# Performance work log

Measured on AMD Instinct MI355X. Metric: run time of the kernel, lower is better.

## Reference

```python
import jax, jax.numpy as jnp
import numpy as np

EPS = 1e-5
TOPK = 4

def bn(x, gamma, beta, mean, var, axis=1):
    # inference-mode batchnorm (running stats)
    shp = [1] * x.ndim
    shp[axis] = -1
    scale = (gamma / jnp.sqrt(var + EPS)).reshape(shp)
    shift = (beta - mean * gamma / jnp.sqrt(var + EPS)).reshape(shp)
    return x * scale + shift


def setup_inputs() -> dict:
    key = jax.random.key(0)
    ks = jax.random.split(key, 4)
    B, C, T, H, W = 8, 512, 8, 28, 28
    R = 64
    Cq = C // 4
    s = 0.05
    return {
        "input": jax.random.normal(ks[0], (B, C, T, H, W), dtype=jnp.float32),
        "w_reduce": jax.random.normal(ks[1], (R, C), dtype=jnp.float32) * s,
        "bn1_gamma": jnp.ones((R,), jnp.float32), "bn1_beta": jnp.zeros((R,), jnp.float32),
        "bn1_mean": jnp.zeros((R,), jnp.float32), "bn1_var": jnp.ones((R,), jnp.float32),
        "w_proj": jax.random.normal(ks[2], (Cq, C + 2), dtype=jnp.float32) * s,
        "bn2_gamma": jnp.ones((Cq,), jnp.float32), "bn2_beta": jnp.zeros((Cq,), jnp.float32),
        "bn2_mean": jnp.zeros((Cq,), jnp.float32), "bn2_var": jnp.ones((Cq,), jnp.float32),
        "w_t": jax.random.normal(ks[3], (C, Cq, 3, 1), dtype=jnp.float32) * s,
        "bn3_gamma": jnp.ones((C,), jnp.float32), "bn3_beta": jnp.zeros((C,), jnp.float32),
        "bn3_mean": jnp.zeros((C,), jnp.float32), "bn3_var": jnp.ones((C,), jnp.float32),
    }


def reference(input, w_reduce, bn1_gamma, bn1_beta, bn1_mean, bn1_var,
              w_proj, bn2_gamma, bn2_beta, bn2_mean, bn2_var,
              w_t, bn3_gamma, bn3_beta, bn3_mean, bn3_var):
    x = input
    B, C, T, H, W = x.shape
    R = w_reduce.shape[0]
    K = TOPK
    HW = H * W

    # spatial template from frame 0
    template_d = x[:, :, 0].reshape(B, C, HW)                                  # (B,C,HW)
    template_p = bn(jnp.einsum('rc,bcs->brs', w_reduce, template_d),
                    bn1_gamma, bn1_beta, bn1_mean, bn1_var)                     # (B,R,HW)
    spt_inds = jnp.argmax(template_p, axis=2)                                  # (B,R)
    template_resample = jnp.take_along_axis(template_d, spt_inds[:, None, :], axis=2)  # (B,C,R)

    x_flat = x.reshape(B, C, T * HW)
    affinity = jnp.einsum('bcr,bcs->brs', template_resample, x_flat)           # (B,R,T*HW)
    affinity = affinity.reshape(B, R, T, HW)
    _, topk_inds = jax.lax.top_k(affinity, K)                                  # (B,R,T,K)
    inds = jnp.transpose(topk_inds, (0, 3, 2, 1))                              # (B,K,T,R)

    # gather trajectory features: traj[b,k,c,t,r] = x[b,c,t, inds[b,k,t,r]]
    x4 = x.reshape(B, C, T, HW)
    traj = jnp.take_along_axis(x4[:, None], inds[:, :, None], axis=4)          # (B,K,C,T,R)
    traj_bk = traj.reshape(B * K, C, T, R)

    inds_bk = inds.reshape(B * K, 1, T, R)
    row = (inds_bk // W).astype(jnp.float32) / H
    col = (inds_bk % W).astype(jnp.float32) / W
    coords = jnp.concatenate([row, col], axis=1)                               # (B*K,2,T,R)

    fuse = jnp.concatenate([traj_bk, coords], axis=1)                          # (B*K,C+2,T,R)
    fuse = bn(jnp.einsum('qc,bctr->bqtr', w_proj, fuse),
              bn2_gamma, bn2_beta, bn2_mean, bn2_var)                          # (B*K,C/4,T,R)
    fuse = fuse.reshape(B, K, C // 4, T, R).max(axis=1)                        # (B,C/4,T,R)

    tc = jax.lax.conv_general_dilated(fuse, w_t, window_strides=(1, 1),
                                      padding=((1, 1), (0, 0)),
                                      dimension_numbers=('NCHW', 'OIHW', 'NCHW'))
    tc = jax.nn.relu(bn(tc, bn3_gamma, bn3_beta, bn3_mean, bn3_var))           # (B,C,T,R)

    points = traj.mean(axis=1).reshape(B, C, T * R)                            # (B,C,T*R)
    proj = jnp.einsum('bcp,bcs->bps', points, x_flat)                          # (B,T*R,T*HW)
    proj = jax.nn.softmax(proj, axis=1)                                        # softmax over T*R (dim=1)
    prop = jnp.einsum('bcp,bps->bcs', tc.reshape(B, C, T * R), proj)           # (B,C,T*HW)
    return x + prop.reshape(B, C, T, H, W)
```

## Files before the change

### kernel.cpp

```cpp
#include <hip/hip_runtime.h>

#define EPSB 1e-5f

#define B_   8
#define C_   512
#define T_   8
#define HW_  784
#define S_   6272
#define R_   64
#define CQ_  128
#define K_   4
#define P_   512

typedef _Float16 f16;
typedef __attribute__((ext_vector_type(8))) _Float16 f16x8;
typedef __attribute__((ext_vector_type(4))) _Float16 f16x4;
typedef __attribute__((ext_vector_type(4))) float    f32x4;

#define OB_PTST  0ull
#define OB_TC    4194304ull
#define OB_D     8388608ull
#define OB_TRH   8589312ull
#define OB_TRF   9113600ull
#define OB_INDS  10162176ull
#define OB_WRH   10227712ull
#define OB_WPH   10293248ull
#define OB_WTH   10424320ull
#define OB_XT    10817536ull
#define T_TPA    62197760ull
#define T_AFF    63803392ull
#define T_FUSEK  62197760ull
#define T_FUSE   66392064ull
#define CHB      62197760ull

#define SBAR()  __builtin_amdgcn_s_barrier()
#define SCHB()  __builtin_amdgcn_sched_barrier(0)
#define WAITV(N) asm volatile("s_waitcnt vmcnt(" #N ")" ::: "memory")

__device__ __forceinline__ void gload16(const void* g, void* l) {
    __builtin_amdgcn_global_load_lds(
        (const __attribute__((address_space(1))) unsigned int*)g,
        (__attribute__((address_space(3))) unsigned int*)l, 16, 0, 0);
}

__global__ __launch_bounds__(256) void k_prep(
    const float* __restrict__ wr, const float* __restrict__ wp,
    const float* __restrict__ wt,
    f16* __restrict__ wrh, f16* __restrict__ wph, f16* __restrict__ wth)
{
    int i = blockIdx.x*256 + threadIdx.x;
    if (i < 32768) {
        wrh[i] = (f16)wr[i];
    } else if (i < 98304) {
        int j = i - 32768;
        int q = j >> 9, c = j & 511;
        wph[j] = (f16)wp[q*514 + c];
    } else {
        int j = i - 98304;
        int co = j / 384;
        int rem = j - co*384;
        int dt = rem >> 7, ci = rem & 127;
        wth[j] = (f16)wt[(size_t)(co*CQ_ + ci)*3 + dt];
    }
}

__global__ __launch_bounds__(256) void k_xpose(
    const float* __restrict__ x, f16* __restrict__ xT)
{
    __shared__ float tile[64][65];
    int s0 = blockIdx.x*64, c0 = blockIdx.y*64, b = blockIdx.z;
    int tid = threadIdx.x;
    #pragma unroll
    for (int i = 0; i < 4; ++i) {
        int idx = tid + i*256;
        int cl = idx >> 4, s4 = (idx & 15)*4;
        f32x4 v = *(const f32x4*)&x[((size_t)(b*C_ + c0+cl))*S_ + s0 + s4];
        tile[cl][s4] = v.x; tile[cl][s4+1] = v.y;
        tile[cl][s4+2] = v.z; tile[cl][s4+3] = v.w;
    }
    __syncthreads();
    #pragma unroll
    for (int i = 0; i < 4; ++i) {
        int idx = tid + i*256;
        int sl = idx >> 4, c4 = (idx & 15)*4;
        f16x4 h;
        h[0] = (f16)tile[c4+0][sl]; h[1] = (f16)tile[c4+1][sl];
        h[2] = (f16)tile[c4+2][sl]; h[3] = (f16)tile[c4+3][sl];
        *(f16x4*)&xT[((size_t)(b*S_ + s0+sl))*C_ + c0 + c4] = h;
    }
}

__global__ __launch_bounds__(256) void k_templ(
    const f16* __restrict__ xT, const f16* __restrict__ wrh,
    float* __restrict__ tpa)
{
    __shared__ __align__(16) f16 As[2][128*64];
    __shared__ __align__(16) f16 Bs[2][64*64];
    int b = blockIdx.y; int s0 = blockIdx.x*128;
    int tid = threadIdx.x;
    int lane = tid & 63, w = tid >> 6;
    int lrow = lane >> 3;
    int swzc = ((lane & 7) ^ lrow) * 8;
    const f16* ga = xT  + ((size_t)b*S_ + s0 + w*32 + lrow)*C_ + swzc;
    const f16* gb = wrh + (size_t)(w*16 + lrow)*C_ + swzc;
    int mbase = (w & 1)*64, nbase = (w >> 1)*32;
    int fr = lane & 15, quad = lane >> 4;
    int sw = fr & 7;
    f32x4 acc[4][2] = {};
    #pragma unroll
    for (int j = 0; j < 4; ++j)
        gload16(ga + j*8*C_, &As[0][(w*32 + j*8)*64]);
    #pragma unroll
    for (int j = 0; j < 2; ++j)
        gload16(gb + j*8*C_, &Bs[0][(w*16 + j*8)*64]);
    ga += 64; gb += 64;
    int cur = 0;
    for (int i = 0; i < 8; ++i) {
        if (i < 7) {
            #pragma unroll
            for (int j = 0; j < 4; ++j)
                gload16(ga + j*8*C_, &As[cur^1][(w*32 + j*8)*64]);
            #pragma unroll
            for (int j = 0; j < 2; ++j)
                gload16(gb + j*8*C_, &Bs[cur^1][(w*16 + j*8)*64]);
            ga += 64; gb += 64;
            WAITV(6);
        } else {
            WAITV(0);
        }
        SCHB(); SBAR();
        #pragma unroll
        for (int kk = 0; kk < 2; ++kk) {
            int ch = ((kk*4 + quad) ^ sw) * 8;
            f16x8 af[4], bf[2];
            #pragma unroll
            for (int mt = 0; mt < 4; ++mt)
                af[mt] = *(const f16x8*)&As[cur][(mbase + mt*16 + fr)*64 + ch];
            #pragma unroll
            for (int nt = 0; nt < 2; ++nt)
                bf[nt] = *(const f16x8*)&Bs[cur][(nbase + nt*16 + fr)*64 + ch];
            #pragma unroll
            for (int mt = 0; mt < 4; ++mt)
                #pragma unroll
                for (int nt = 0; nt < 2; ++nt)
                    acc[mt][nt] = __builtin_amdgcn_mfma_f32_16x16x32_f16(
                        af[mt], bf[nt], acc[mt][nt], 0, 0, 0);
        }
        SBAR();
        cur ^= 1;
    }
    #pragma unroll
    for (int mt = 0; mt < 4; ++mt) {
        int sb = s0 + mbase + mt*16 + quad*4;
        if (sb < HW_) {
            #pragma unroll
            for (int nt = 0; nt < 2; ++nt) {
                int r = nbase + nt*16 + fr;
                *(f32x4*)&tpa[((size_t)(b*R_ + r))*HW_ + sb] = acc[mt][nt];
            }
        }
    }
}

__global__ __launch_bounds__(256) void k_targmax(
    const float* __restrict__ x, const float* __restrict__ wr_g,
    const float* __restrict__ g1, const float* __restrict__ v1,
    const float* __restrict__ tpa,
    float* __restrict__ trf, f16* __restrict__ trh)
{
    __shared__ float row[HW_];
    __shared__ float sval[256];
    __shared__ int   sidx[256];
    __shared__ float cval[4];
    __shared__ int   cidx[4];
    __shared__ float eval_[4];
    __shared__ int   bestind;
    int bid = blockIdx.x;
    int b = bid >> 6, r = bid & 63;
    int tid = threadIdx.x;
    float sc = g1[r] * rsqrtf(v1[r] + EPSB);
    const float* tprow = tpa + (size_t)bid*HW_;
    for (int s = tid; s < HW_; s += 256) row[s] = tprow[s]*sc;
    __syncthreads();
    for (int pass = 0; pass < 4; ++pass) {
        float best = -INFINITY; int bi = 0;
        for (int s = tid; s < HW_; s += 256) {
            float v = row[s];
            if (v > best) { best = v; bi = s; }
        }
        sval[tid] = best; sidx[tid] = bi;
        __syncthreads();
        for (int off = 128; off > 0; off >>= 1) {
            if (tid < off) {
                float ov = sval[tid+off]; int oi = sidx[tid+off];
                if (ov > sval[tid] || (ov == sval[tid] && oi < sidx[tid])) {
                    sval[tid] = ov; sidx[tid] = oi;
                }
            }
            __syncthreads();
        }
        if (tid == 0) {
            cval[pass] = sval[0]; cidx[pass] = sidx[0];
            row[sidx[0]] = -INFINITY;
        }
        __syncthreads();
    }
    float thr = 0.05f * fabsf(sc);
    if (cval[0] - cval[1] >= thr) {
        if (tid == 0) bestind = cidx[0];
    } else {
        int w = tid >> 6, lane = tid & 63;
        int cand = cidx[w];
        float sum = 0.f;
        #pragma unroll
        for (int i = 0; i < 8; ++i) {
            int c = lane + i*64;
            sum += wr_g[r*C_ + c] * x[((size_t)(b*C_ + c))*S_ + cand];
        }
        #pragma unroll
        for (int off = 32; off > 0; off >>= 1) sum += __shfl_xor(sum, off);
        if (lane == 0) eval_[w] = sum*sc;
        __syncthreads();
        if (tid == 0) {
            float bv = eval_[0]; int bi2 = cidx[0];
            for (int j = 1; j < 4; ++j) {
                float v = eval_[j]; int ii = cidx[j];
                if (v > bv || (v == bv && ii < bi2)) { bv = v; bi2 = ii; }
            }
            bestind = bi2;
        }
    }
    __syncthreads();
    int ind = bestind;
    for (int c = tid; c < C_; c += 256) {
        float v = x[((size_t)(b*C_ + c))*S_ + ind];
        trf[(size_t)bid*C_ + c] = v;
        trh[(size_t)bid*C_ + c] = (f16)v;
    }
}

__global__ __launch_bounds__(256) void k_affin(
    const f16* __restrict__ xT, const f16* __restrict__ trh,
    float* __restrict__ aff)
{
    __shared__ __align__(16) f16 As[2][128*64];
    __shared__ __align__(16) f16 Bs[2][64*64];
    int b = blockIdx.y; int s0 = blockIdx.x*128;
    int tid = threadIdx.x;
    int lane = tid & 63, w = tid >> 6;
    int lrow = lane >> 3;
    int swzc = ((lane & 7) ^ lrow) * 8;
    const f16* ga = xT  + ((size_t)b*S_ + s0 + w*32 + lrow)*C_ + swzc;
    const f16* gb = trh + ((size_t)(b*R_) + w*16 + lrow)*C_ + swzc;
    int mbase = (w & 1)*64, nbase = (w >> 1)*32;
    int fr = lane & 15, quad = lane >> 4;
    int sw = fr & 7;
    f32x4 acc[4][2] = {};
    #pragma unroll
    for (int j = 0; j < 4; ++j)
        gload16(ga + j*8*C_, &As[0][(w*32 + j*8)*64]);
    #pragma unroll
    for (int j = 0; j < 2; ++j)
        gload16(gb + j*8*C_, &Bs[0][(w*16 + j*8)*64]);
    ga += 64; gb += 64;
    int cur = 0;
    for (int i = 0; i < 8; ++i) {
        if (i < 7) {
            #pragma unroll
            for (int j = 0; j < 4; ++j)
                gload16(ga + j*8*C_, &As[cur^1][(w*32 + j*8)*64]);
            #pragma unroll
            for (int j = 0; j < 2; ++j)
                gload16(gb + j*8*C_, &Bs[cur^1][(w*16 + j*8)*64]);
            ga += 64; gb += 64;
            WAITV(6);
        } else {
            WAITV(0);
        }
        SCHB(); SBAR();
        #pragma unroll
        for (int kk = 0; kk < 2; ++kk) {
            int ch = ((kk*4 + quad) ^ sw) * 8;
            f16x8 af[4], bf[2];
            #pragma unroll
            for (int mt = 0; mt < 4; ++mt)
                af[mt] = *(const f16x8*)&As[cur][(mbase + mt*16 + fr)*64 + ch];
            #pragma unroll
            for (int nt = 0; nt < 2; ++nt)
                bf[nt] = *(const f16x8*)&Bs[cur][(nbase + nt*16 + fr)*64 + ch];
            #pragma unroll
            for (int mt = 0; mt < 4; ++mt)
                #pragma unroll
                for (int nt = 0; nt < 2; ++nt)
                    acc[mt][nt] = __builtin_amdgcn_mfma_f32_16x16x32_f16(
                        af[mt], bf[nt], acc[mt][nt], 0, 0, 0);
        }
        SBAR();
        cur ^= 1;
    }
    #pragma unroll
    for (int mt = 0; mt < 4; ++mt) {
        int sb = s0 + mbase + mt*16 + quad*4;
        #pragma unroll
        for (int nt = 0; nt < 2; ++nt) {
            int r = nbase + nt*16 + fr;
            *(f32x4*)&aff[((size_t)(b*R_ + r))*S_ + sb] = acc[mt][nt];
        }
    }
}

__global__ __launch_bounds__(256) void k_topk(
    const float* __restrict__ x, const float* __restrict__ trf,
    const float* __restrict__ aff, int* __restrict__ inds)
{
    __shared__ float row[HW_];
    __shared__ float sval[256];
    __shared__ int   sidx[256];
    __shared__ float cval[8];
    __shared__ int   cidx[8];
    __shared__ float eval_[8];
    int r = blockIdx.x, t = blockIdx.y, b = blockIdx.z;
    int tid = threadIdx.x;
    const float* arow = aff + ((size_t)(b*R_ + r))*S_ + t*HW_;
    for (int s = tid; s < HW_; s += 256) row[s] = arow[s];
    __syncthreads();
    for (int pass = 0; pass < 8; ++pass) {
        float best = -INFINITY; int bi = 0;
        for (int s = tid; s < HW_; s += 256) {
            float v = row[s];
            if (v > best) { best = v; bi = s; }
        }
        sval[tid] = best; sidx[tid] = bi;
        __syncthreads();
        for (int off = 128; off > 0; off >>= 1) {
            if (tid < off) {
                float ov = sval[tid+off]; int oi = sidx[tid+off];
                if (ov > sval[tid] || (ov == sval[tid] && oi < sidx[tid])) {
                    sval[tid] = ov; sidx[tid] = oi;
                }
            }
            __syncthreads();
        }
        if (tid == 0) {
            cval[pass] = sval[0]; cidx[pass] = sidx[0];
            row[sidx[0]] = -INFINITY;
        }
        __syncthreads();
    }
    if (cval[3] - cval[4] >= 0.35f) {
        if (tid < K_)
            inds[((b*K_ + tid)*T_ + t)*R_ + r] = cidx[tid];
    } else {
        int w = tid >> 6, lane = tid & 63;
        #pragma unroll
        for (int half = 0; half < 2; ++half) {
            int j = w + half*4;
            int cand = cidx[j];
            float sum = 0.f;
            #pragma unroll
            for (int i = 0; i < 8; ++i) {
                int c = lane + i*64;
                sum += trf[((size_t)(b*R_ + r))*C_ + c]
                     * x[((size_t)(b*C_ + c))*S_ + t*HW_ + cand];
            }
            #pragma unroll
            for (int off = 32; off > 0; off >>= 1) sum += __shfl_xor(sum, off);
            if (lane == 0) eval_[j] = sum;
        }
        __syncthreads();
        if (tid == 0) {
            unsigned used = 0;
            for (int k = 0; k < K_; ++k) {
                float bv = -INFINITY; int bj = -1;
                for (int j = 0; j < 8; ++j) {
                    if (used & (1u << j)) continue;
                    float v = eval_[j]; int ii = cidx[j];
                    if (bj < 0 || v > bv || (v == bv && ii < cidx[bj])) {
                        bv = v; bj = j;
                    }
                }
                used |= 1u << bj;
                inds[((b*K_ + k)*T_ + t)*R_ + r] = cidx[bj];
            }
        }
    }
}

__global__ __launch_bounds__(256) void k_pointsT(
    const float* __restrict__ x, const int* __restrict__ inds,
    f16* __restrict__ ptsT)
{
    __shared__ float tile[64][65];
    __shared__ int   indl[4][64];
    int c0 = blockIdx.x*64, t = blockIdx.y, b = blockIdx.z;
    int tid = threadIdx.x;
    {
        int k = tid >> 6, r = tid & 63;
        indl[k][r] = inds[((b*K_ + k)*T_ + t)*R_ + r];
    }
    __syncthreads();
    #pragma unroll
    for (int i = 0; i < 16; ++i) {
        int idx = tid + i*256;
        int cl = idx >> 6, r = idx & 63;
        const float* base = x + (size_t)(b*C_ + c0 + cl)*S_ + t*HW_;
        float v = base[indl[0][r]] + base[indl[1][r]] + base[indl[2][r]] + base[indl[3][r]];
        tile[cl][r] = 0.25f*v;
    }
    __syncthreads();
    #pragma unroll
    for (int i = 0; i < 16; ++i) {
        int idx = tid + i*256;
        int rl = idx >> 6, cl = idx & 63;
        ptsT[((size_t)b*P_ + t*64 + rl)*C_ + c0 + cl] = (f16)tile[cl][rl];
    }
}

__global__ __launch_bounds__(256) void k_fuse(
    const f16* __restrict__ xT, const f16* __restrict__ wph,
    const float* __restrict__ wp,
    const float* __restrict__ g2, const float* __restrict__ b2,
    const float* __restrict__ m2, const float* __restrict__ v2,
    f16* __restrict__ fusekT, const int* __restrict__ inds)
{
    __shared__ __align__(16) f16 As[2][128*32];
    __shared__ __align__(16) f16 Bs[2][64*32];
    __shared__ float scq[128], shq[128], wrq[128], wcq[128];
    __shared__ float rowv[64], colv[64];
    int bid = blockIdx.x;
    int t = bid & 7, bk = bid >> 3;
    int b = bk >> 2;
    int tid = threadIdx.x;
    int lane = tid & 63, w = tid >> 6;
    if (tid < 128) {
        float sc = g2[tid] * rsqrtf(v2[tid] + EPSB);
        scq[tid] = sc;
        shq[tid] = b2[tid] - m2[tid]*sc;
        wrq[tid] = wp[tid*514 + 512];
        wcq[tid] = wp[tid*514 + 513];
    } else if (tid < 192) {
        int r = tid - 128;
        int id = inds[bk*T_*R_ + t*R_ + r];
        rowv[r] = (float)(id / 28) * (1.0f/28.0f);
        colv[r] = (float)(id % 28) * (1.0f/28.0f);
    }
    int strow = tid >> 2;
    int slot  = (tid & 3) ^ (strow & 3);
    int ind = inds[bk*T_*R_ + t*R_ + strow];
    const f16* ga = wph + (size_t)strow*C_ + slot*8;
    const f16* gb = xT + ((size_t)b*S_ + t*HW_ + ind)*C_ + slot*8;
    int mbase = (w & 1)*64, nbase = (w >> 1)*32;
    int fr = lane & 15, quad = lane >> 4;
    f32x4 acc[4][2] = {};
    __syncthreads();
    gload16(ga,         (f16*)As[0] + tid*8);
    gload16(ga + 64*C_, (f16*)As[0] + 2048 + tid*8);
    gload16(gb,         (f16*)Bs[0] + tid*8);
    ga += 32; gb += 32;
    int cur = 0;
    for (int i = 0; i < 16; ++i) {
        if (i < 15) {
            gload16(ga,         (f16*)As[cur^1] + tid*8);
            gload16(ga + 64*C_, (f16*)As[cur^1] + 2048 + tid*8);
            gload16(gb,         (f16*)Bs[cur^1] + tid*8);
            ga += 32; gb += 32;
            WAITV(3);
        } else {
            WAITV(0);
        }
        SCHB(); SBAR();
        f16x8 af[4], bf[2];
        #pragma unroll
        for (int mt = 0; mt < 4; ++mt) {
            int ar = mbase + mt*16 + fr;
            af[mt] = *(const f16x8*)&As[cur][ar*32 + ((quad ^ (ar & 3))*8)];
        }
        #pragma unroll
        for (int nt = 0; nt < 2; ++nt) {
            int br = nbase + nt*16 + fr;
            bf[nt] = *(const f16x8*)&Bs[cur][br*32 + ((quad ^ (br & 3))*8)];
        }
        #pragma unroll
        for (int mt = 0; mt < 4; ++mt)
            #pragma unroll
            for (int nt = 0; nt < 2; ++nt)
                acc[mt][nt] = __builtin_amdgcn_mfma_f32_16x16x32_f16(
                    af[mt], bf[nt], acc[mt][nt], 0, 0, 0);
        SBAR();
        cur ^= 1;
    }
    #pragma unroll
    for (int mt = 0; mt < 4; ++mt) {
        int qb = mbase + mt*16 + quad*4;
        #pragma unroll
        for (int nt = 0; nt < 2; ++nt) {
            int r = nbase + nt*16 + fr;
            f16x4 h;
            #pragma unroll
            for (int i = 0; i < 4; ++i) {
                int q = qb + i;
                float v = acc[mt][nt][i] + wrq[q]*rowv[r] + wcq[q]*colv[r];
                h[i] = (f16)(v*scq[q] + shq[q]);
            }
            *(f16x4*)&fusekT[((size_t)bk*P_ + t*R_ + r)*CQ_ + qb] = h;
        }
    }
}

__global__ __launch_bounds__(256) void k_maxk(
    const f16* __restrict__ fusekT, f16* __restrict__ fuseT)
{
    int idx8 = (blockIdx.x*256 + threadIdx.x)*8;
    int b = idx8 >> 16;
    int pq = idx8 & 65535;
    const f16* base = fusekT + (size_t)(b*4)*65536 + pq;
    f16x8 v0 = *(const f16x8*)base;
    #pragma unroll
    for (int k = 1; k < K_; ++k) {
        f16x8 vk = *(const f16x8*)(base + (size_t)k*65536);
        #pragma unroll
        for (int j = 0; j < 8; ++j)
            v0[j] = (float)vk[j] > (float)v0[j] ? vk[j] : v0[j];
    }
    *(f16x8*)&fuseT[(size_t)b*65536 + pq] = v0;
}

__global__ __launch_bounds__(256) void k_conv(
    const f16* __restrict__ wth,
    const float* __restrict__ g3, const float* __restrict__ b3,
    const float* __restrict__ m3, const float* __restrict__ v3,
    const f16* __restrict__ fuseT, f16* __restrict__ tc)
{
    __shared__ __align__(16) f16 As[128*64];
    __shared__ __align__(16) f16 Bs[128*64];
    int p0 = blockIdx.x*128, c0 = blockIdx.y*128, b = blockIdx.z;
    int tid = threadIdx.x;
    int lane = tid & 63, w = tid >> 6;
    int lrow = lane >> 3;
    int swzc = ((lane & 7) ^ lrow) * 8;
    int mrow = (w & 1)*64, nrow = (w >> 1)*64;
    int fr = lane & 15, quad = lane >> 4;
    int sw = fr & 7;
    f32x4 acc[4][4] = {};
    for (int step = 0; step < 6; ++step) {
        int dt = step >> 1, h = step & 1;
        int shift = (dt - 1)*64;
        #pragma unroll
        for (int j = 0; j < 4; ++j) {
            int rb = w*32 + j*8;
            int pg = p0 + rb + shift;
            if (pg >= 0 && pg < P_)
                gload16(fuseT + ((size_t)b*P_ + pg + lrow)*CQ_ + h*64 + swzc,
                        &As[rb*64]);
            else
                *(f32x4*)((char*)&As[rb*64] + lane*16) = (f32x4){0.f,0.f,0.f,0.f};
        }
        #pragma unroll
        for (int j = 0; j < 4; ++j) {
            int rb = w*32 + j*8;
            gload16(wth + (size_t)(c0 + rb + lrow)*384 + dt*128 + h*64 + swzc,
                    &Bs[rb*64]);
        }
        __syncthreads();
        #pragma unroll
        for (int kk = 0; kk < 2; ++kk) {
            int ch = ((kk*4 + quad) ^ sw) * 8;
            f16x8 af[4], bf[4];
            #pragma unroll
            for (int mt = 0; mt < 4; ++mt)
                af[mt] = *(const f16x8*)&As[(mrow + mt*16 + fr)*64 + ch];
            #pragma unroll
            for (int nt = 0; nt < 4; ++nt)
                bf[nt] = *(const f16x8*)&Bs[(nrow + nt*16 + fr)*64 + ch];
            #pragma unroll
            for (int mt = 0; mt < 4; ++mt)
                #pragma unroll
                for (int nt = 0; nt < 4; ++nt)
                    acc[mt][nt] = __builtin_amdgcn_mfma_f32_16x16x32_f16(
                        af[mt], bf[nt], acc[mt][nt], 0, 0, 0);
        }
        __syncthreads();
    }
    #pragma unroll
    for (int nt = 0; nt < 4; ++nt) {
        int co = c0 + nrow + nt*16 + fr;
        float sc = g3[co] * rsqrtf(v3[co] + EPSB);
        float sh = b3[co] - m3[co]*sc;
        #pragma unroll
        for (int mt = 0; mt < 4; ++mt) {
            int p = p0 + mrow + mt*16 + quad*4;
            f16x4 hv;
            #pragma unroll
            for (int i = 0; i < 4; ++i)
                hv[i] = (f16)fmaxf(acc[mt][nt][i]*sc + sh, 0.f);
            *(f16x4*)&tc[((size_t)(b*C_ + co))*P_ + p] = hv;
        }
    }
}

__global__ __launch_bounds__(512, 2) void k_attnW(
    const f16* __restrict__ xT, const f16* __restrict__ ptsT,
    f16* __restrict__ W, float* __restrict__ Dinv, int st, int NCHb)
{
    __shared__ __align__(16) f16 As[2][128*32];
    __shared__ __align__(16) f16 Bs[2][512*32];
    int lt = blockIdx.x; int b = blockIdx.z;
    int s0 = (st + lt)*128;
    int tid = threadIdx.x;
    int lane = tid & 63, w = tid >> 6;
    int wr = w & 1, wc = w >> 1;
    int strow = tid >> 2;
    int slot  = (tid & 3) ^ (strow & 3);
    const f16* ga = xT   + ((size_t)b*S_ + s0 + strow)*C_ + slot*8;
    const f16* gb = ptsT + ((size_t)b*P_ + strow)*C_ + slot*8;
    int fr = lane & 15, quad = lane >> 4;
    f32x4 acc[8][4] = {};
    gload16(ga, (f16*)As[0] + tid*8);
    #pragma unroll
    for (int j = 0; j < 4; ++j)
        gload16(gb + (size_t)j*128*C_, (f16*)Bs[0] + j*4096 + tid*8);
    ga += 32; gb += 32;
    int cur = 0;
    for (int i = 0; i < 16; ++i) {
        if (i < 15) {
            gload16(ga, (f16*)As[cur^1] + tid*8);
            #pragma unroll
            for (int j = 0; j < 4; ++j)
                gload16(gb + (size_t)j*128*C_, (f16*)Bs[cur^1] + j*4096 + tid*8);
            ga += 32; gb += 32;
            WAITV(5);
        } else {
            WAITV(0);
        }
        SCHB(); SBAR();
        f16x8 af[4], bf[8];
        #pragma unroll
        for (int mt = 0; mt < 4; ++mt) {
            int ar = wr*64 + mt*16 + fr;
            af[mt] = *(const f16x8*)&As[cur][ar*32 + ((quad ^ (ar & 3))*8)];
        }
        #pragma unroll
        for (int nt = 0; nt < 8; ++nt) {
            int br = wc*128 + nt*16 + fr;
            bf[nt] = *(const f16x8*)&Bs[cur][br*32 + ((quad ^ (br & 3))*8)];
        }
        #pragma unroll
        for (int nt = 0; nt < 8; ++nt)
            #pragma unroll
            for (int mt = 0; mt < 4; ++mt)
                acc[nt][mt] = __builtin_amdgcn_mfma_f32_16x16x32_f16(
                    bf[nt], af[mt], acc[nt][mt], 0, 0, 0);
        SBAR();
        cur ^= 1;
    }
    float (*red)[4] = (float (*)[4])As;
    float M[4];
    #pragma unroll
    for (int mt = 0; mt < 4; ++mt) {
        float m = -INFINITY;
        #pragma unroll
        for (int nt = 0; nt < 8; ++nt)
            #pragma unroll
            for (int i = 0; i < 4; ++i)
                m = fmaxf(m, acc[nt][mt][i]);
        m = fmaxf(m, __shfl_xor(m, 16));
        m = fmaxf(m, __shfl_xor(m, 32));
        if (quad == 0) red[wr*64 + mt*16 + fr][wc] = m;
    }
    __syncthreads();
    #pragma unroll
    for (int mt = 0; mt < 4; ++mt) {
        int srow = wr*64 + mt*16 + fr;
        M[mt] = fmaxf(fmaxf(red[srow][0], red[srow][1]),
                      fmaxf(red[srow][2], red[srow][3]));
    }
    __syncthreads();
    #pragma unroll
    for (int mt = 0; mt < 4; ++mt) {
        float s = 0.f;
        #pragma unroll
        for (int nt = 0; nt < 8; ++nt)
            #pragma unroll
            for (int i = 0; i < 4; ++i) {
                float e = __expf(acc[nt][mt][i] - M[mt]);
                acc[nt][mt][i] = e;
                s += e;
            }
        s += __shfl_xor(s, 16);
        s += __shfl_xor(s, 32);
        if (quad == 0) red[wr*64 + mt*16 + fr][wc] = s;
    }
    __syncthreads();
    size_t wbase = (size_t)(b*NCHb + lt)*128*(size_t)P_;
    #pragma unroll
    for (int mt = 0; mt < 4; ++mt) {
        int srow = wr*64 + mt*16 + fr;
        float tot = (red[srow][0] + red[srow][1]) + (red[srow][2] + red[srow][3]);
        if (wc == 0 && quad == 0)
            Dinv[(size_t)b*S_ + s0 + srow] = 1.0f/tot;
        #pragma unroll
        for (int nt = 0; nt < 8; ++nt) {
            f16x4 h;
            #pragma unroll
            for (int i = 0; i < 4; ++i) h[i] = (f16)acc[nt][mt][i];
            *(f16x4*)&W[wbase + (size_t)srow*P_ + wc*128 + nt*16 + quad*4] = h;
        }
    }
}

__global__ __launch_bounds__(256) void k_gemmP(
    const f16* __restrict__ tc, const f16* __restrict__ W,
    const float* __restrict__ Dinv, const float* __restrict__ x,
    float* __restrict__ out, int st, int NCHb)
{
    __shared__ __align__(16) f16 As[2][128*64];
    __shared__ __align__(16) f16 Bs[2][128*64];
    int lt = blockIdx.x; int b = blockIdx.z;
    int s0 = (st + lt)*128, c0t = blockIdx.y*128;
    int tid = threadIdx.x;
    int lane = tid & 63, w = tid >> 6;
    int lrow = lane >> 3;
    int swzc = ((lane & 7) ^ lrow) * 8;
    const f16* ga = tc + ((size_t)(b*C_) + c0t + w*32 + lrow)*P_ + swzc;
    const f16* gb = W  + ((size_t)(b*NCHb + lt)*128 + w*32 + lrow)*P_ + swzc;
    int mrow = (w & 1)*64, nrow = (w >> 1)*64;
    int fr = lane & 15, quad = lane >> 4;
    int sw = fr & 7;
    f32x4 acc[4][4] = {};
    #pragma unroll
    for (int j = 0; j < 4; ++j)
        gload16(ga + j*8*P_, &As[0][(w*32 + j*8)*64]);
    #pragma unroll
    for (int j = 0; j < 4; ++j)
        gload16(gb + j*8*P_, &Bs[0][(w*32 + j*8)*64]);
    ga += 64; gb += 64;
    int cur = 0;
    for (int i = 0; i < 8; ++i) {
        if (i < 7) {
            #pragma unroll
            for (int j = 0; j < 4; ++j)
                gload16(ga + j*8*P_, &As[cur^1][(w*32 + j*8)*64]);
            #pragma unroll
            for (int j = 0; j < 4; ++j)
                gload16(gb + j*8*P_, &Bs[cur^1][(w*32 + j*8)*64]);
            ga += 64; gb += 64;
            WAITV(8);
        } else {
            WAITV(0);
        }
        SCHB(); SBAR();
        #pragma unroll
        for (int kk = 0; kk < 2; ++kk) {
            int ch = ((kk*4 + quad) ^ sw) * 8;
            f16x8 af[4], bf[4];
            #pragma unroll
            for (int mt = 0; mt < 4; ++mt)
                af[mt] = *(const f16x8*)&As[cur][(mrow + mt*16 + fr)*64 + ch];
            #pragma unroll
            for (int nt = 0; nt < 4; ++nt)
                bf[nt] = *(const f16x8*)&Bs[cur][(nrow + nt*16 + fr)*64 + ch];
            #pragma unroll
            for (int nt = 0; nt < 4; ++nt)
                #pragma unroll
                for (int mt = 0; mt < 4; ++mt)
                    acc[nt][mt] = __builtin_amdgcn_mfma_f32_16x16x32_f16(
                        bf[nt], af[mt], acc[nt][mt], 0, 0, 0);
        }
        SBAR();
        cur ^= 1;
    }
    #pragma unroll
    for (int nt = 0; nt < 4; ++nt) {
        int s = s0 + nrow + nt*16 + quad*4;
        f32x4 dv = *(const f32x4*)&Dinv[(size_t)b*S_ + s];
        #pragma unroll
        for (int mt = 0; mt < 4; ++mt) {
            int c = c0t + mrow + mt*16 + fr;
            size_t o = ((size_t)(b*C_ + c))*S_ + s;
            f32x4 xv = *(const f32x4*)&x[o];
            f32x4 res = xv + acc[nt][mt]*dv;
            *(f32x4*)&out[o] = res;
        }
    }
}

extern "C" void kernel_launch(void* const* d_in, const int* in_sizes, int n_in,
                              void* d_out, int out_size, void* d_ws, size_t ws_size,
                              hipStream_t stream) {
    const float* x   = (const float*)d_in[0];
    const float* wrd = (const float*)d_in[1];
    const float* g1  = (const float*)d_in[2];
    const float* v1  = (const float*)d_in[5];
    const float* wp  = (const float*)d_in[6];
    const float* g2  = (const float*)d_in[7];
    const float* b2  = (const float*)d_in[8];
    const float* m2  = (const float*)d_in[9];
    const float* v2  = (const float*)d_in[10];
    const float* wt  = (const float*)d_in[11];
    const float* g3  = (const float*)d_in[12];
    const float* b3  = (const float*)d_in[13];
    const float* m3  = (const float*)d_in[14];
    const float* v3  = (const float*)d_in[15];
    char*  wsb = (char*)d_ws;
    float* out = (float*)d_out;

    f16*   ptsT  = (f16*)  (wsb + OB_PTST);
    f16*   tc    = (f16*)  (wsb + OB_TC);
    float* Dinv  = (float*)(wsb + OB_D);
    f16*   trh   = (f16*)  (wsb + OB_TRH);
    float* trf   = (float*)(wsb + OB_TRF);
    int*   inds  = (int*)  (wsb + OB_INDS);
    f16*   wrh   = (f16*)  (wsb + OB_WRH);
    f16*   wph   = (f16*)  (wsb + OB_WPH);
    f16*   wth   = (f16*)  (wsb + OB_WTH);
    f16*   xT    = (f16*)  (wsb + OB_XT);
    float* tpa   = (float*)(wsb + T_TPA);
    float* aff   = (float*)(wsb + T_AFF);
    f16*   fusekT= (f16*)  (wsb + T_FUSEK);
    f16*   fuseT = (f16*)  (wsb + T_FUSE);

    const size_t PER_TILE = 1048576ull;
    size_t avail = ws_size > CHB ? ws_size - CHB : 0;
    int NCH = (int)(avail / PER_TILE);
    if (NCH < 1) NCH = 1;
    if (NCH > 49) NCH = 49;
    int nchunks = (49 + NCH - 1)/NCH;
    int NCHb = (49 + nchunks - 1)/nchunks;
    f16* W = (f16*)(wsb + CHB);

    k_prep<<<1152, 256, 0, stream>>>(wrd, wp, wt, wrh, wph, wth);
    k_xpose<<<dim3(98, 8, 8), 256, 0, stream>>>(x, xT);
    k_templ<<<dim3(7, 8), 256, 0, stream>>>(xT, wrh, tpa);
    k_targmax<<<512, 256, 0, stream>>>(x, wrd, g1, v1, tpa, trf, trh);
    k_affin<<<dim3(49, 8), 256, 0, stream>>>(xT, trh, aff);
    k_topk<<<dim3(R_, T_, B_), 256, 0, stream>>>(x, trf, aff, inds);
    k_pointsT<<<dim3(8, 8, 8), 256, 0, stream>>>(x, inds, ptsT);
    k_fuse<<<256, 256, 0, stream>>>(xT, wph, wp, g2, b2, m2, v2, fusekT, inds);
    k_maxk<<<256, 256, 0, stream>>>(fusekT, fuseT);
    k_conv<<<dim3(4, 4, 8), 256, 0, stream>>>(wth, g3, b3, m3, v3, fuseT, tc);

    for (int st = 0; st < 49; st += NCHb) {
        int cnt = (49 - st) < NCHb ? (49 - st) : NCHb;
        k_attnW<<<dim3(cnt, 1, 8), 512, 0, stream>>>(xT, ptsT, W, Dinv, st, NCHb);
        k_gemmP<<<dim3(cnt, 4, 8), 256, 0, stream>>>(tc, W, Dinv, x, out, st, NCHb);
    }
}
```

Measured before the change: 480.4 us.

## Fuse softmax-weight and propagation GEMMs into one kernel keeping weights in LDS

Merges the attention-weight kernel and the propagation GEMM into a single kernel. Each block computes its 128x512 softmax weight tile, keeps it in about 147KB of LDS with a swizzled layout, then loops over all 512 channels multiplying by streamed tc tiles and writing x + prop. This removes the global round trip of the f16 weight matrix and the normalizer array, along with the chunked launch loop. In exchange only 392 blocks run at one block per CU because of the LDS footprint, so occupancy drops and the second GEMM uses small 2x2 MFMA tiles per wave.

```diff
diff --git a/kernel.cpp b/kernel.cpp
--- a/kernel.cpp
+++ b/kernel.cpp
@@ -31,7 +31,6 @@
 #define T_AFF    63803392ull
 #define T_FUSEK  62197760ull
 #define T_FUSE   66392064ull
-#define CHB      62197760ull
 
 #define SBAR()  __builtin_amdgcn_s_barrier()
 #define SCHB()  __builtin_amdgcn_sched_barrier(0)
@@ -598,188 +597,190 @@
     }
 }
 
-__global__ __launch_bounds__(512, 2) void k_attnW(
+__global__ __launch_bounds__(512, 2) void k_attnP(
     const f16* __restrict__ xT, const f16* __restrict__ ptsT,
-    f16* __restrict__ W, float* __restrict__ Dinv, int st, int NCHb)
-{
-    __shared__ __align__(16) f16 As[2][128*32];
-    __shared__ __align__(16) f16 Bs[2][512*32];
-    int lt = blockIdx.x; int b = blockIdx.z;
-    int s0 = (st + lt)*128;
+    const f16* __restrict__ tc, const float* __restrict__ x,
+    float* __restrict__ out)
+{
+    __shared__ __align__(16) char ldsb[150016];
+    f16*  P1A  = (f16*)ldsb;
+    f16*  P1B  = (f16*)(ldsb + 16384);
+    f16*  Wl   = (f16*)ldsb;
+    f16*  TCs  = (f16*)(ldsb + 131072);
+    float* dinv = (float*)(ldsb + 147456);
+    float (*red)[4] = (float (*)[4])(ldsb + 147968);
+
+    int lt = blockIdx.x, b = blockIdx.y;
+    int s0 = lt*128;
     int tid = threadIdx.x;
     int lane = tid & 63, w = tid >> 6;
     int wr = w & 1, wc = w >> 1;
-    int strow = tid >> 2;
-    int slot  = (tid & 3) ^ (strow & 3);
-    const f16* ga = xT   + ((size_t)b*S_ + s0 + strow)*C_ + slot*8;
-    const f16* gb = ptsT + ((size_t)b*P_ + strow)*C_ + slot*8;
     int fr = lane & 15, quad = lane >> 4;
-    f32x4 acc[8][4] = {};
-    gload16(ga, (f16*)As[0] + tid*8);
-    #pragma unroll
-    for (int j = 0; j < 4; ++j)
-        gload16(gb + (size_t)j*128*C_, (f16*)Bs[0] + j*4096 + tid*8);
-    ga += 32; gb += 32;
-    int cur = 0;
-    for (int i = 0; i < 16; ++i) {
-        if (i < 15) {
-            gload16(ga, (f16*)As[cur^1] + tid*8);
-            #pragma unroll
-            for (int j = 0; j < 4; ++j)
-                gload16(gb + (size_t)j*128*C_, (f16*)Bs[cur^1] + j*4096 + tid*8);
-            ga += 32; gb += 32;
-            WAITV(5);
-        } else {
-            WAITV(0);
-        }
-        SCHB(); SBAR();
-        f16x8 af[4], bf[8];
-        #pragma unroll
-        for (int mt = 0; mt < 4; ++mt) {
-            int ar = wr*64 + mt*16 + fr;
-            af[mt] = *(const f16x8*)&As[cur][ar*32 + ((quad ^ (ar & 3))*8)];
-        }
-        #pragma unroll
-        for (int nt = 0; nt < 8; ++nt) {
-            int br = wc*128 + nt*16 + fr;
-            bf[nt] = *(const f16x8*)&Bs[cur][br*32 + ((quad ^ (br & 3))*8)];
-        }
-        #pragma unroll
-        for (int nt = 0; nt < 8; ++nt)
-            #pragma unroll
-            for (int mt = 0; mt < 4; ++mt)
-                acc[nt][mt] = __builtin_amdgcn_mfma_f32_16x16x32_f16(
-                    bf[nt], af[mt], acc[nt][mt], 0, 0, 0);
-        SBAR();
-        cur ^= 1;
-    }
-    float (*red)[4] = (float (*)[4])As;
-    float M[4];
-    #pragma unroll
-    for (int mt = 0; mt < 4; ++mt) {
-        float m = -INFINITY;
-        #pragma unroll
-        for (int nt = 0; nt < 8; ++nt)
-            #pragma unroll
-            for (int i = 0; i < 4; ++i)
-                m = fmaxf(m, acc[nt][mt][i]);
-        m = fmaxf(m, __shfl_xor(m, 16));
-        m = fmaxf(m, __shfl_xor(m, 32));
-        if (quad == 0) red[wr*64 + mt*16 + fr][wc] = m;
-    }
-    __syncthreads();
-    #pragma unroll
-    for (int mt = 0; mt < 4; ++mt) {
-        int srow = wr*64 + mt*16 + fr;
-        M[mt] = fmaxf(fmaxf(red[srow][0], red[srow][1]),
-                      fmaxf(red[srow][2], red[srow][3]));
-    }
-    __syncthreads();
-    #pragma unroll
-    for (int mt = 0; mt < 4; ++mt) {
-        float s = 0.f;
-        #pragma unroll
-        for (int nt = 0; nt < 8; ++nt)
-            #pragma unroll
-            for (int i = 0; i < 4; ++i) {
-                float e = __expf(acc[nt][mt][i] - M[mt]);
-                acc[nt][mt][i] = e;
-                s += e;
-            }
-        s += __shfl_xor(s, 16);
-        s += __shfl_xor(s, 32);
-        if (quad == 0) red[wr*64 + mt*16 + fr][wc] = s;
-    }
-    __syncthreads();
-    size_t wbase = (size_t)(b*NCHb + lt)*128*(size_t)P_;
-    #pragma unroll
-    for (int mt = 0; mt < 4; ++mt) {
-        int srow = wr*64 + mt*16 + fr;
-        float tot = (red[srow][0] + red[srow][1]) + (red[srow][2] + red[srow][3]);
-        if (wc == 0 && quad == 0)
-            Dinv[(size_t)b*S_ + s0 + srow] = 1.0f/tot;
-        #pragma unroll
-        for (int nt = 0; nt < 8; ++nt) {
-            f16x4 h;
-            #pragma unroll
-            for (int i = 0; i < 4; ++i) h[i] = (f16)acc[nt][mt][i];
-            *(f16x4*)&W[wbase + (size_t)srow*P_ + wc*128 + nt*16 + quad*4] = h;
-        }
-    }
-}
-
-__global__ __launch_bounds__(256) void k_gemmP(
-    const f16* __restrict__ tc, const f16* __restrict__ W,
-    const float* __restrict__ Dinv, const float* __restrict__ x,
-    float* __restrict__ out, int st, int NCHb)
-{
-    __shared__ __align__(16) f16 As[2][128*64];
-    __shared__ __align__(16) f16 Bs[2][128*64];
-    int lt = blockIdx.x; int b = blockIdx.z;
-    int s0 = (st + lt)*128, c0t = blockIdx.y*128;
-    int tid = threadIdx.x;
-    int lane = tid & 63, w = tid >> 6;
-    int lrow = lane >> 3;
-    int swzc = ((lane & 7) ^ lrow) * 8;
-    const f16* ga = tc + ((size_t)(b*C_) + c0t + w*32 + lrow)*P_ + swzc;
-    const f16* gb = W  + ((size_t)(b*NCHb + lt)*128 + w*32 + lrow)*P_ + swzc;
-    int mrow = (w & 1)*64, nrow = (w >> 1)*64;
-    int fr = lane & 15, quad = lane >> 4;
-    int sw = fr & 7;
-    f32x4 acc[4][4] = {};
-    #pragma unroll
-    for (int j = 0; j < 4; ++j)
-        gload16(ga + j*8*P_, &As[0][(w*32 + j*8)*64]);
-    #pragma unroll
-    for (int j = 0; j < 4; ++j)
-        gload16(gb + j*8*P_, &Bs[0][(w*32 + j*8)*64]);
-    ga += 64; gb += 64;
-    int cur = 0;
-    for (int i = 0; i < 8; ++i) {
-        if (i < 7) {
-            #pragma unroll
-            for (int j = 0; j < 4; ++j)
-                gload16(ga + j*8*P_, &As[cur^1][(w*32 + j*8)*64]);
-            #pragma unroll
-            for (int j = 0; j < 4; ++j)
-                gload16(gb + j*8*P_, &Bs[cur^1][(w*32 + j*8)*64]);
-            ga += 64; gb += 64;
-            WAITV(8);
-        } else {
-            WAITV(0);
-        }
-        SCHB(); SBAR();
-        #pragma unroll
-        for (int kk = 0; kk < 2; ++kk) {
-            int ch = ((kk*4 + quad) ^ sw) * 8;
-            f16x8 af[4], bf[4];
-            #pragma unroll
-            for (int mt = 0; mt < 4; ++mt)
-                af[mt] = *(const f16x8*)&As[cur][(mrow + mt*16 + fr)*64 + ch];
-            #pragma unroll
-            for (int nt = 0; nt < 4; ++nt)
-                bf[nt] = *(const f16x8*)&Bs[cur][(nrow + nt*16 + fr)*64 + ch];
-            #pragma unroll
-            for (int nt = 0; nt < 4; ++nt)
+
+    {
+        int strow = tid >> 2;
+        int slot  = (tid & 3) ^ (strow & 3);
+        const f16* ga = xT   + ((size_t)b*S_ + s0 + strow)*C_ + slot*8;
+        const f16* gb = ptsT + ((size_t)b*P_ + strow)*C_ + slot*8;
+        f32x4 acc[8][4] = {};
+        gload16(ga, P1A + tid*8);
+        #pragma unroll
+        for (int j = 0; j < 4; ++j)
+            gload16(gb + (size_t)j*128*C_, P1B + j*4096 + tid*8);
+        ga += 32; gb += 32;
+        int cur = 0;
+        for (int i = 0; i < 16; ++i) {
+            if (i < 15) {
+                gload16(ga, P1A + (cur^1)*4096 + tid*8);
+                #pragma unroll
+                for (int j = 0; j < 4; ++j)
+                    gload16(gb + (size_t)j*128*C_, P1B + (cur^1)*16384 + j*4096 + tid*8);
+                ga += 32; gb += 32;
+                WAITV(5);
+            } else {
+                WAITV(0);
+            }
+            SCHB(); SBAR();
+            f16x8 af[4], bf[8];
+            #pragma unroll
+            for (int mt = 0; mt < 4; ++mt) {
+                int ar = wr*64 + mt*16 + fr;
+                af[mt] = *(const f16x8*)&P1A[cur*4096 + ar*32 + ((quad ^ (ar & 3))*8)];
+            }
+            #pragma unroll
+            for (int nt = 0; nt < 8; ++nt) {
+                int br = wc*128 + nt*16 + fr;
+                bf[nt] = *(const f16x8*)&P1B[cur*16384 + br*32 + ((quad ^ (br & 3))*8)];
+            }
+            #pragma unroll
+            for (int nt = 0; nt < 8; ++nt)
                 #pragma unroll
                 for (int mt = 0; mt < 4; ++mt)
                     acc[nt][mt] = __builtin_amdgcn_mfma_f32_16x16x32_f16(
                         bf[nt], af[mt], acc[nt][mt], 0, 0, 0);
-        }
-        SBAR();
-        cur ^= 1;
-    }
-    #pragma unroll
-    for (int nt = 0; nt < 4; ++nt) {
-        int s = s0 + nrow + nt*16 + quad*4;
-        f32x4 dv = *(const f32x4*)&Dinv[(size_t)b*S_ + s];
+            SBAR();
+            cur ^= 1;
+        }
+        float M[4];
         #pragma unroll
         for (int mt = 0; mt < 4; ++mt) {
-            int c = c0t + mrow + mt*16 + fr;
-            size_t o = ((size_t)(b*C_ + c))*S_ + s;
-            f32x4 xv = *(const f32x4*)&x[o];
-            f32x4 res = xv + acc[nt][mt]*dv;
-            *(f32x4*)&out[o] = res;
+            float m = -INFINITY;
+            #pragma unroll
+            for (int nt = 0; nt < 8; ++nt)
+                #pragma unroll
+                for (int i = 0; i < 4; ++i)
+                    m = fmaxf(m, acc[nt][mt][i]);
+            m = fmaxf(m, __shfl_xor(m, 16));
+            m = fmaxf(m, __shfl_xor(m, 32));
+            if (quad == 0) red[wr*64 + mt*16 + fr][wc] = m;
+        }
+        __syncthreads();
+        #pragma unroll
+        for (int mt = 0; mt < 4; ++mt) {
+            int srow = wr*64 + mt*16 + fr;
+            M[mt] = fmaxf(fmaxf(red[srow][0], red[srow][1]),
+                          fmaxf(red[srow][2], red[srow][3]));
+        }
+        __syncthreads();
+        #pragma unroll
+        for (int mt = 0; mt < 4; ++mt) {
+            float s = 0.f;
+            #pragma unroll
+            for (int nt = 0; nt < 8; ++nt)
+                #pragma unroll
+                for (int i = 0; i < 4; ++i) {
+                    float e = __expf(acc[nt][mt][i] - M[mt]);
+                    acc[nt][mt][i] = e;
+                    s += e;
+                }
+            s += __shfl_xor(s, 16);
+            s += __shfl_xor(s, 32);
+            if (quad == 0) red[wr*64 + mt*16 + fr][wc] = s;
+        }
+        __syncthreads();
+        #pragma unroll
+        for (int mt = 0; mt < 4; ++mt) {
+            int srow = wr*64 + mt*16 + fr;
+            float tot = (red[srow][0] + red[srow][1]) + (red[srow][2] + red[srow][3]);
+            if (wc == 0 && quad == 0)
+                dinv[srow] = 1.0f/tot;
+            #pragma unroll
+            for (int nt = 0; nt < 8; ++nt) {
+                f16x4 h;
+                #pragma unroll
+                for (int i = 0; i < 4; ++i) h[i] = (f16)acc[nt][mt][i];
+                int p0 = wc*128 + nt*16 + quad*4;
+                int g  = p0 >> 3;
+                int gp = (g & ~7) | ((g & 7) ^ (srow & 7));
+                *(f16x4*)&Wl[srow*512 + gp*8 + (quad & 1)*4] = h;
+            }
+        }
+    }
+    __syncthreads();
+
+    int cgrp = w >> 2;
+    int sgrp = w & 3;
+    int tr = tid >> 3;
+    int tslot = (tid & 7) ^ (tr & 7);
+    for (int c0 = 0; c0 < C_; c0 += 64) {
+        const f16* gtc = tc + ((size_t)(b*C_) + c0 + tr)*P_ + tslot*8;
+        f32x4 xv2[2][2], dv2[2], acc2[2][2];
+        #pragma unroll
+        for (int nt2 = 0; nt2 < 2; ++nt2) {
+            int s = sgrp*32 + nt2*16 + quad*4;
+            dv2[nt2] = *(const f32x4*)&dinv[s];
+            #pragma unroll
+            for (int mt2 = 0; mt2 < 2; ++mt2) {
+                int c = c0 + cgrp*32 + mt2*16 + fr;
+                xv2[nt2][mt2] = *(const f32x4*)&x[((size_t)(b*C_ + c))*S_ + s0 + s];
+                acc2[nt2][mt2] = (f32x4){0.f,0.f,0.f,0.f};
+            }
+        }
+        gload16(gtc, TCs + tid*8);
+        gtc += 64;
+        int cur2 = 0;
+        for (int i2 = 0; i2 < 8; ++i2) {
+            if (i2 < 7) {
+                gload16(gtc, TCs + (cur2^1)*4096 + tid*8);
+                gtc += 64;
+                WAITV(1);
+            } else {
+                WAITV(0);
+            }
+            SCHB(); SBAR();
+            #pragma unroll
+            for (int kk = 0; kk < 2; ++kk) {
+                f16x8 af2[2], bf2[2];
+                #pragma unroll
+                for (int mt2 = 0; mt2 < 2; ++mt2) {
+                    int ar = cgrp*32 + mt2*16 + fr;
+                    af2[mt2] = *(const f16x8*)&TCs[cur2*4096 + ar*64 + ((kk*4 + quad) ^ (ar & 7))*8];
+                }
+                #pragma unroll
+                for (int nt2 = 0; nt2 < 2; ++nt2) {
+                    int br = sgrp*32 + nt2*16 + fr;
+                    int gp = i2*8 + ((kk*4 + quad) ^ (br & 7));
+                    bf2[nt2] = *(const f16x8*)&Wl[br*512 + gp*8];
+                }
+                #pragma unroll
+                for (int nt2 = 0; nt2 < 2; ++nt2)
+                    #pragma unroll
+                    for (int mt2 = 0; mt2 < 2; ++mt2)
+                        acc2[nt2][mt2] = __builtin_amdgcn_mfma_f32_16x16x32_f16(
+                            bf2[nt2], af2[mt2], acc2[nt2][mt2], 0, 0, 0);
+            }
+            SBAR();
+            cur2 ^= 1;
+        }
+        #pragma unroll
+        for (int nt2 = 0; nt2 < 2; ++nt2) {
+            int s = sgrp*32 + nt2*16 + quad*4;
+            #pragma unroll
+            for (int mt2 = 0; mt2 < 2; ++mt2) {
+                int c = c0 + cgrp*32 + mt2*16 + fr;
+                size_t o = ((size_t)(b*C_ + c))*S_ + s0 + s;
+                *(f32x4*)&out[o] = xv2[nt2][mt2] + acc2[nt2][mt2]*dv2[nt2];
+            }
         }
     }
 }
@@ -806,7 +807,6 @@
 
     f16*   ptsT  = (f16*)  (wsb + OB_PTST);
     f16*   tc    = (f16*)  (wsb + OB_TC);
-    float* Dinv  = (float*)(wsb + OB_D);
     f16*   trh   = (f16*)  (wsb + OB_TRH);
     float* trf   = (float*)(wsb + OB_TRF);
     int*   inds  = (int*)  (wsb + OB_INDS);
@@ -819,15 +819,6 @@
     f16*   fusekT= (f16*)  (wsb + T_FUSEK);
     f16*   fuseT = (f16*)  (wsb + T_FUSE);
 
-    const size_t PER_TILE = 1048576ull;
-    size_t avail = ws_size > CHB ? ws_size - CHB : 0;
-    int NCH = (int)(avail / PER_TILE);
-    if (NCH < 1) NCH = 1;
-    if (NCH > 49) NCH = 49;
-    int nchunks = (49 + NCH - 1)/NCH;
-    int NCHb = (49 + nchunks - 1)/nchunks;
-    f16* W = (f16*)(wsb + CHB);
-
     k_prep<<<1152, 256, 0, stream>>>(wrd, wp, wt, wrh, wph, wth);
     k_xpose<<<dim3(98, 8, 8), 256, 0, stream>>>(x, xT);
     k_templ<<<dim3(7, 8), 256, 0, stream>>>(xT, wrh, tpa);
@@ -838,10 +829,5 @@
     k_fuse<<<256, 256, 0, stream>>>(xT, wph, wp, g2, b2, m2, v2, fusekT, inds);
     k_maxk<<<256, 256, 0, stream>>>(fusekT, fuseT);
     k_conv<<<dim3(4, 4, 8), 256, 0, stream>>>(wth, g3, b3, m3, v3, fuseT, tc);
-
-    for (int st = 0; st < 49; st += NCHb) {
-        int cnt = (49 - st) < NCHb ? (49 - st) : NCHb;
-        k_attnW<<<dim3(cnt, 1, 8), 512, 0, stream>>>(xT, ptsT, W, Dinv, st, NCHb);
-        k_gemmP<<<dim3(cnt, 4, 8), 256, 0, stream>>>(tc, W, Dinv, x, out, st, NCHb);
-    }
-}
+    k_attnP<<<dim3(49, 8), 512, 0, stream>>>(xT, ptsT, tc, x, out);
+}
```

After: 454.6 us. 5.4% less time.
